# Optimization experiments

Measured on AMD Instinct MI355X. Metric: run time of the kernel, lower is better.

Reference implementation:

```python
import jax, jax.numpy as jnp
import numpy as np
from jax import lax

B, T, V, E, H, C, K = 256, 512, 50000, 128, 256, 128, 2


def setup_inputs() -> dict:
    key = jax.random.key(0)
    ks = jax.random.split(key, 16)
    s = lambda *sh: 1.0 / np.sqrt(sh[0])
    return {
        "input_current": jax.random.randint(ks[0], (B, T), 0, V, dtype=jnp.int32),
        "input_left": jax.random.randint(ks[1], (B, T), 0, V, dtype=jnp.int32),
        "input_right": jax.random.randint(ks[2], (B, T), 0, V, dtype=jnp.int32),
        "emb": jax.random.normal(ks[3], (V, E), jnp.float32) * 0.05,
        "Wf": jax.random.normal(ks[4], (E, H), jnp.float32) * s(E),
        "Uf": jax.random.normal(ks[5], (H, H), jnp.float32) * s(H),
        "bf": jnp.zeros((H,), jnp.float32),
        "Wb": jax.random.normal(ks[6], (E, H), jnp.float32) * s(E),
        "Ub": jax.random.normal(ks[7], (H, H), jnp.float32) * s(H),
        "bb": jnp.zeros((H,), jnp.float32),
        "Wc": jax.random.normal(ks[8], (2 * H + E, C), jnp.float32) * s(2 * H + E),
        "bc": jnp.zeros((C,), jnp.float32),
        "Wd": jax.random.normal(ks[9], (C, K), jnp.float32) * s(C),
        "bd": jnp.zeros((K,), jnp.float32),
    }


def _simple_rnn(x, W, U, b):
    # x: [B,T,E] -> outputs [B,T,H]; h_t = tanh(x_t W + b + h_{t-1} U)
    xw = jnp.einsum("bte,eh->bth", x, W) + b  # precompute input projection
    h0 = jnp.zeros((x.shape[0], U.shape[0]), x.dtype)

    def step(h, xw_t):
        h = jnp.tanh(xw_t + h @ U)
        return h, h

    _, hs = lax.scan(step, h0, jnp.swapaxes(xw, 0, 1))  # scan over time
    return jnp.swapaxes(hs, 0, 1)


def reference(input_current, input_left, input_right, emb, Wf, Uf, bf, Wb, Ub, bb, Wc, bc, Wd, bd):
    e_cur = emb[input_current]  # [B,T,E]
    e_left = emb[input_left]
    e_right = emb[input_right]
    x_left = _simple_rnn(e_left, Wf, Uf, bf)  # [B,T,H]
    # go_backwards RNN: process reversed sequence, then model reverses back
    x_right = _simple_rnn(e_right[:, ::-1], Wb, Ub, bb)[:, ::-1]  # [B,T,H]
    x = jnp.concatenate([x_left, e_cur, x_right], axis=2)  # [B,T,2H+E]
    x = jnp.tanh(jnp.einsum("btd,dc->btc", x, Wc) + bc)  # Conv1D k=1 + tanh
    x = jnp.max(x, axis=1)  # GlobalMaxPooling1D
    return jax.nn.sigmoid(x @ Wd + bd)  # [B,K]
```

## Files before the change

kernel.cpp:

```cpp
#include <hip/hip_runtime.h>
#include <hip/hip_bf16.h>


#define B_ 256
#define T_ 512
#define E_ 128
#define H_ 256
#define C_ 128

typedef __attribute__((ext_vector_type(8))) short short8;
typedef __attribute__((ext_vector_type(4))) float float4v;
typedef __attribute__((ext_vector_type(2))) unsigned int uint2v;

__device__ inline unsigned short f2bf(float f) {
  unsigned u = __float_as_uint(f);
  u += 0x7fffu + ((u >> 16) & 1u);
  return (unsigned short)(u >> 16);
}
__device__ inline unsigned pkbf(float a, float b) {
  __hip_bfloat162 h2 = __float22bfloat162_rn(float2{a, b});
  union { __hip_bfloat162 h; unsigned u; } cv;
  cv.h = h2;
  return cv.u;
}
__device__ inline float lo16f(unsigned u) { return __uint_as_float(u << 16); }
__device__ inline float hi16f(unsigned u) { return __uint_as_float(u & 0xffff0000u); }
__device__ inline float fast_tanh(float x) {
  float e = __expf(2.f * x);
  float r = __builtin_amdgcn_rcpf(e + 1.f);
  return __builtin_fmaf(-2.f, r, 1.f);
}
__device__ inline unsigned enc_f(float f) {
  unsigned u = __float_as_uint(f);
  return (u & 0x80000000u) ? ~u : (u | 0x80000000u);
}
__device__ inline float dec_f(unsigned key) {
  unsigned bits = (key & 0x80000000u) ? (key ^ 0x80000000u) : ~key;
  return __uint_as_float(bits);
}
__device__ inline void sync_lds() {
  asm volatile("s_waitcnt lgkmcnt(0)\n\ts_barrier" ::: "memory");
}

__global__ __launch_bounds__(256) void prep_kernel(
    const float* __restrict__ Wf, const float* __restrict__ Wb,
    const float* __restrict__ Wc, const float* __restrict__ Uf,
    const float* __restrict__ Ub,
    unsigned short* __restrict__ WfT, unsigned short* __restrict__ WbT,
    unsigned short* __restrict__ WcT, unsigned short* __restrict__ UfT,
    unsigned short* __restrict__ UbT) {
  int gid = blockIdx.x * 256 + threadIdx.x;
  int stride = gridDim.x * 256;
  for (int i = gid; i < 128 * 256; i += stride) {
    int k = i >> 8, n = i & 255;
    WfT[n * 128 + k] = f2bf(Wf[i]);
    WbT[n * 128 + k] = f2bf(Wb[i]);
  }
  for (int i = gid; i < 640 * 128; i += stride) {
    int k = i >> 7, n = i & 127;
    WcT[n * 640 + k] = f2bf(Wc[i]);
  }
  for (int i = gid; i < 256 * 256; i += stride) {
    int k = i >> 8, n = i & 255;
    UfT[n * 256 + k] = f2bf(Uf[i]);
    UbT[n * 256 + k] = f2bf(Ub[i]);
  }
}

__global__ __launch_bounds__(256) void embxw_kernel(
    const int* __restrict__ idxL, const int* __restrict__ idxR,
    const int* __restrict__ idxC, const float* __restrict__ emb,
    const unsigned short* __restrict__ WfT, const unsigned short* __restrict__ WbT,
    const float* __restrict__ bfv, const float* __restrict__ bbv,
    unsigned short* __restrict__ x) {
  const int dir = blockIdx.z;
  const int t0 = blockIdx.x * 4;
  const int b0 = blockIdx.y * 16;
  const int tid = threadIdx.x;
  const int w = tid >> 6, lane = tid & 63, q = lane >> 4, l15 = lane & 15;

  if (dir == 2) {
    const int t = t0 + w;
    const int er = idxC[(b0 + l15) * T_ + t];
    const float* ep = emb + (size_t)er * E_;
#pragma unroll
    for (int u = 0; u < 8; ++u) {
      float4v a = *(const float4v*)(ep + 16 * u + 4 * q);
      uint2v pk = {pkbf(a[0], a[1]), pkbf(a[2], a[3])};
      int row = b0 + u + 8 * (q >> 1);
      *(uint2v*)(x + ((size_t)row * T_ + t) * 640 + 256 + 64 * (q & 1) +
                 4 * l15) = pk;
    }
    return;
  }

  const int* __restrict__ idx = dir ? idxR : idxL;
  const unsigned short* __restrict__ WT = dir ? WbT : WfT;
  const float* __restrict__ bias = dir ? bbv : bfv;

  short8 wfr[4][4];
#pragma unroll
  for (int mt = 0; mt < 4; ++mt)
#pragma unroll
    for (int kt = 0; kt < 4; ++kt)
      wfr[mt][kt] = *(const short8*)(WT + (64 * w + 16 * mt + l15) * 128 +
                                     kt * 32 + q * 8);
  float4v bv[4];
#pragma unroll
  for (int mt = 0; mt < 4; ++mt)
    bv[mt] = *(const float4v*)(bias + 64 * w + 16 * mt + 4 * q);

#pragma unroll 1
  for (int j = 0; j < 4; ++j) {
    const int t = t0 + j;
    const int er = idx[(b0 + l15) * T_ + t];
    const float* ep = emb + (size_t)er * E_;
    short8 efr[4];
#pragma unroll
    for (int kt = 0; kt < 4; ++kt) {
      const float* p8 = ep + kt * 32 + q * 8;
      float4v a0 = *(const float4v*)p8;
      float4v a1 = *(const float4v*)(p8 + 4);
      union { unsigned u[4]; short8 s; } cv;
      cv.u[0] = pkbf(a0[0], a0[1]);
      cv.u[1] = pkbf(a0[2], a0[3]);
      cv.u[2] = pkbf(a1[0], a1[1]);
      cv.u[3] = pkbf(a1[2], a1[3]);
      efr[kt] = cv.s;
    }
    float4v acc[4];
#pragma unroll
    for (int mt = 0; mt < 4; ++mt) acc[mt] = (float4v){0.f, 0.f, 0.f, 0.f};
#pragma unroll
    for (int kt = 0; kt < 4; ++kt)
#pragma unroll
      for (int mt = 0; mt < 4; ++mt)
        acc[mt] = __builtin_amdgcn_mfma_f32_16x16x32_bf16(wfr[mt][kt], efr[kt],
                                                          acc[mt], 0, 0, 0);
#pragma unroll
    for (int mt = 0; mt < 4; ++mt) {
      float4v v = acc[mt] + bv[mt];
      uint2v pk = {pkbf(v[0], v[1]), pkbf(v[2], v[3])};
      *(uint2v*)(x + ((size_t)(b0 + 4 * w + mt) * T_ + t) * 640 + dir * 384 +
                 lane * 4) = pk;
    }
  }
}

__global__ __launch_bounds__(512, 2) void rnn_kernel(
    unsigned short* x, const unsigned short* __restrict__ UfT,
    const unsigned short* __restrict__ UbT) {
  const int dir = blockIdx.x & 1;
  const int b0 = (blockIdx.x >> 1) * 16;
  const unsigned short* __restrict__ UT = dir ? UbT : UfT;
  const int xoff = dir ? 384 : 0;
  const int tstep = dir ? -1 : 1;
  const int t0 = dir ? (T_ - 1) : 0;
  const ptrdiff_t dstep = (ptrdiff_t)tstep * 640;

  const int tid = threadIdx.x;
  const int wv = tid >> 6, lane = tid & 63, q = lane >> 4, l15 = lane & 15;

  __shared__ __attribute__((aligned(16))) unsigned short hbuf[2][16][280];
  unsigned short* hb0 = &hbuf[0][0][0];
  unsigned short* hb1 = &hbuf[1][0][0];

  for (int i = tid; i < 16 * 280; i += 512) hb0[i] = 0;

  short8 ufr[2][8];
#pragma unroll
  for (int mt = 0; mt < 2; ++mt)
#pragma unroll
    for (int kt = 0; kt < 8; ++kt)
      ufr[mt][kt] = *(const short8*)(UT + (32 * wv + 16 * mt + l15) * H_ +
                                     kt * 32 + q * 8);

  unsigned short* ptrS[2];
  const unsigned short* ptrL[2];
  uint2v curA[2], curB[2], infA[2], infB[2];
#pragma unroll
  for (int mt = 0; mt < 2; ++mt) {
    unsigned short* base =
        x + (size_t)(b0 + 2 * wv + mt) * T_ * 640 + xoff + lane * 4;
    unsigned short* bt = base + (ptrdiff_t)t0 * 640;
    curA[mt] = *(const uint2v*)(bt);
    curB[mt] = *(const uint2v*)(bt + dstep);
    infA[mt] = *(const uint2v*)(bt + 2 * dstep);
    infB[mt] = *(const uint2v*)(bt + 3 * dstep);
    ptrS[mt] = bt;
    ptrL[mt] = bt + 4 * dstep;
  }

  const unsigned lrd = l15 * 280;
  const unsigned lwr = l15 * 280 + 32 * wv;

  __syncthreads();

#pragma unroll 1
  for (int p = 0; p < 256; ++p) {
    uint2v ldA[2], ldB[2];
    if (p < 254) {
#pragma unroll
      for (int mt = 0; mt < 2; ++mt) {
        ldA[mt] = *(const uint2v*)(ptrL[mt]);
        ldB[mt] = *(const uint2v*)(ptrL[mt] + dstep);
      }
    } else {
#pragma unroll
      for (int mt = 0; mt < 2; ++mt) { ldA[mt] = infA[mt]; ldB[mt] = infB[mt]; }
    }
#pragma unroll
    for (int mt = 0; mt < 2; ++mt) ptrL[mt] += 2 * dstep;

    {
      short8 afr[8];
#pragma unroll
      for (int kt = 0; kt < 8; ++kt)
        afr[kt] = *(const short8*)(hb0 + lrd + kt * 32 + q * 8);
      float4v acc[2];
#pragma unroll
      for (int mt = 0; mt < 2; ++mt)
        acc[mt] = (float4v){lo16f(curA[mt].x), hi16f(curA[mt].x),
                            lo16f(curA[mt].y), hi16f(curA[mt].y)};
#pragma unroll
      for (int kt = 0; kt < 8; ++kt)
#pragma unroll
        for (int mt = 0; mt < 2; ++mt)
          acc[mt] = __builtin_amdgcn_mfma_f32_16x16x32_bf16(
              ufr[mt][kt], afr[kt], acc[mt], 0, 0, 0);
#pragma unroll
      for (int mt = 0; mt < 2; ++mt) {
        uint2v hv = {pkbf(fast_tanh(acc[mt][0]), fast_tanh(acc[mt][1])),
                     pkbf(fast_tanh(acc[mt][2]), fast_tanh(acc[mt][3]))};
        *(uint2v*)(hb1 + lwr + 16 * mt + 4 * q) = hv;
        *(uint2v*)ptrS[mt] = hv;
      }
    }
    sync_lds();

    {
      short8 afr[8];
#pragma unroll
      for (int kt = 0; kt < 8; ++kt)
        afr[kt] = *(const short8*)(hb1 + lrd + kt * 32 + q * 8);
      float4v acc[2];
#pragma unroll
      for (int mt = 0; mt < 2; ++mt)
        acc[mt] = (float4v){lo16f(curB[mt].x), hi16f(curB[mt].x),
                            lo16f(curB[mt].y), hi16f(curB[mt].y)};
#pragma unroll
      for (int kt = 0; kt < 8; ++kt)
#pragma unroll
        for (int mt = 0; mt < 2; ++mt)
          acc[mt] = __builtin_amdgcn_mfma_f32_16x16x32_bf16(
              ufr[mt][kt], afr[kt], acc[mt], 0, 0, 0);
#pragma unroll
      for (int mt = 0; mt < 2; ++mt) {
        uint2v hv = {pkbf(fast_tanh(acc[mt][0]), fast_tanh(acc[mt][1])),
                     pkbf(fast_tanh(acc[mt][2]), fast_tanh(acc[mt][3]))};
        *(uint2v*)(hb0 + lwr + 16 * mt + 4 * q) = hv;
        *(uint2v*)(ptrS[mt] + dstep) = hv;
      }
    }
#pragma unroll
    for (int mt = 0; mt < 2; ++mt) {
      ptrS[mt] += 2 * dstep;
      curA[mt] = infA[mt];
      curB[mt] = infB[mt];
      infA[mt] = ldA[mt];
      infB[mt] = ldB[mt];
    }
    sync_lds();
  }
}

__global__ __launch_bounds__(256, 2) void convpool_kernel(
    const unsigned short* __restrict__ x, const unsigned short* __restrict__ WcT,
    const float* __restrict__ bc, unsigned int* __restrict__ pooled) {
  const int b0 = (blockIdx.x & 15) * 16;
  const int t0 = (blockIdx.x >> 4) * 16;
  const int tid = threadIdx.x;
  const int w = tid >> 6, lane = tid & 63, q = lane >> 4, l15 = lane & 15;

  __shared__ __attribute__((aligned(16))) unsigned short tile[2][16][648];

  short8 wfr[2][20];
#pragma unroll
  for (int ct = 0; ct < 2; ++ct)
#pragma unroll
    for (int kt = 0; kt < 20; ++kt)
      wfr[ct][kt] = *(const short8*)(WcT +
                                     (size_t)(32 * w + 16 * ct + l15) * 640 +
                                     kt * 32 + q * 8);
  float4v bv[2];
#pragma unroll
  for (int ct = 0; ct < 2; ++ct)
    bv[ct] = *(const float4v*)(bc + 32 * w + 16 * ct + 4 * q);

  float4v mx[2];
  mx[0] = (float4v){-1e30f, -1e30f, -1e30f, -1e30f};
  mx[1] = mx[0];

  const int srow = tid >> 4, ssub = tid & 15;
  {
    const unsigned short* src = x + ((size_t)(b0 + srow) * T_ + t0) * 640;
#pragma unroll
    for (int j = 0; j < 5; ++j)
      *(short8*)&tile[0][srow][ssub * 8 + j * 128] =
          *(const short8*)(src + ssub * 8 + j * 128);
  }
  __syncthreads();

#pragma unroll 1
  for (int j = 0; j < 16; ++j) {
    const int t = t0 + j;
    const int buf = j & 1;
    if (j < 15) {
      const unsigned short* src = x + ((size_t)(b0 + srow) * T_ + t + 1) * 640;
#pragma unroll
      for (int jj = 0; jj < 5; ++jj)
        *(short8*)&tile[buf ^ 1][srow][ssub * 8 + jj * 128] =
            *(const short8*)(src + ssub * 8 + jj * 128);
    }
    float4v acc[2];
    acc[0] = (float4v){0.f, 0.f, 0.f, 0.f};
    acc[1] = (float4v){0.f, 0.f, 0.f, 0.f};
#pragma unroll
    for (int kt = 0; kt < 20; ++kt) {
      int row, so1, so2;
      if (kt < 8) {
        row = 2 * kt + (q >> 1);
        so1 = 64 * (2 * (q & 1)) + 4 * l15;
        so2 = so1 + 64;
      } else if (kt < 12) {
        row = 2 * (kt - 8) + (q >> 1) + 8 * (q & 1);
        so1 = 256 + 4 * l15;
        so2 = 320 + 4 * l15;
      } else {
        row = 2 * (kt - 12) + (q >> 1);
        so1 = 384 + 64 * (2 * (q & 1)) + 4 * l15;
        so2 = so1 + 64;
      }
      union { unsigned u[4]; short8 s; } cv;
      uint2v c1 = *(const uint2v*)&tile[buf][row][so1];
      uint2v c2 = *(const uint2v*)&tile[buf][row][so2];
      cv.u[0] = c1.x; cv.u[1] = c1.y; cv.u[2] = c2.x; cv.u[3] = c2.y;
      acc[0] = __builtin_amdgcn_mfma_f32_16x16x32_bf16(wfr[0][kt], cv.s,
                                                       acc[0], 0, 0, 0);
      acc[1] = __builtin_amdgcn_mfma_f32_16x16x32_bf16(wfr[1][kt], cv.s,
                                                       acc[1], 0, 0, 0);
    }
#pragma unroll
    for (int ct = 0; ct < 2; ++ct)
#pragma unroll
      for (int i = 0; i < 4; ++i)
        mx[ct][i] = fmaxf(mx[ct][i], acc[ct][i]);
    __syncthreads();
  }
#pragma unroll
  for (int ct = 0; ct < 2; ++ct)
#pragma unroll
    for (int i = 0; i < 4; ++i)
      atomicMax(pooled + (b0 + l15) * C_ + 32 * w + 16 * ct + 4 * q + i,
                enc_f(fast_tanh(mx[ct][i] + bv[ct][i])));
}

__global__ __launch_bounds__(256) void dense_kernel(
    const unsigned int* __restrict__ pooled, const float* __restrict__ Wd,
    const float* __restrict__ bd, float* __restrict__ out) {
  int b = threadIdx.x;
  float s0 = bd[0], s1 = bd[1];
#pragma unroll 4
  for (int c = 0; c < C_; ++c) {
    float f = dec_f(pooled[b * C_ + c]);
    s0 += f * Wd[c * 2 + 0];
    s1 += f * Wd[c * 2 + 1];
  }
  out[b * 2 + 0] = 1.f / (1.f + __expf(-s0));
  out[b * 2 + 1] = 1.f / (1.f + __expf(-s1));
}

extern "C" void kernel_launch(void* const* d_in, const int* in_sizes, int n_in,
                              void* d_out, int out_size, void* d_ws, size_t ws_size,
                              hipStream_t stream) {
  const int* idxC = (const int*)d_in[0];
  const int* idxL = (const int*)d_in[1];
  const int* idxR = (const int*)d_in[2];
  const float* emb = (const float*)d_in[3];
  const float* Wf = (const float*)d_in[4];
  const float* Uf = (const float*)d_in[5];
  const float* bf_ = (const float*)d_in[6];
  const float* Wb = (const float*)d_in[7];
  const float* Ub = (const float*)d_in[8];
  const float* bb_ = (const float*)d_in[9];
  const float* Wc = (const float*)d_in[10];
  const float* bc = (const float*)d_in[11];
  const float* Wd = (const float*)d_in[12];
  const float* bd = (const float*)d_in[13];

  char* ws = (char*)d_ws;
  unsigned short* x = (unsigned short*)ws;
  unsigned int* pooled = (unsigned int*)(ws + 167772160);
  unsigned short* WfT = (unsigned short*)(ws + 167772160 + 131072);
  unsigned short* WbT = WfT + 256 * 128;
  unsigned short* WcT = WbT + 256 * 128;
  unsigned short* UfT = WcT + 128 * 640;
  unsigned short* UbT = UfT + 256 * 256;

  hipMemsetAsync(pooled, 0, B_ * C_ * sizeof(unsigned int), stream);
  prep_kernel<<<64, 256, 0, stream>>>(Wf, Wb, Wc, Uf, Ub, WfT, WbT, WcT, UfT, UbT);
  embxw_kernel<<<dim3(128, 16, 3), 256, 0, stream>>>(idxL, idxR, idxC, emb,
                                                     WfT, WbT, bf_, bb_, x);
  rnn_kernel<<<32, 512, 0, stream>>>(x, UfT, UbT);
  convpool_kernel<<<512, 256, 0, stream>>>(x, WcT, bc, pooled);
  dense_kernel<<<1, 256, 0, stream>>>(pooled, Wd, bd, (float*)d_out);
}
```

Measured before the change: 629.8 us.

## Precompute vocab projections and fuse conv partial sums into the RNN loop

Projects the whole embedding table through Wf, Wb and the center slice of Wc once (V x 640 table), so the RNN gathers precomputed input projections by token index instead of reading a B x T x 640 activation buffer. The RNN kernel also applies its half of the Conv1D weights to each hidden state as it is produced and writes compact per-direction partial outputs. A lightweight pool kernel then sums the partials with the gathered center term, takes the max over time and applies tanh. This removes the large intermediate write and read and the separate conv GEMM, at the cost of a vocab-sized GEMM, extra MFMAs on the serial RNN critical path, and pre-activation partials rounded to bf16 before they are summed.

New measurement: 713.1 us. 13.2% more time.

```diff
diff --git a/kernel.cpp b/kernel.cpp
--- a/kernel.cpp
+++ b/kernel.cpp
@@ -7,6 +7,7 @@
 #define E_ 128
 #define H_ 256
 #define C_ 128
+#define V_ 50000
 
 typedef __attribute__((ext_vector_type(8))) short short8;
 typedef __attribute__((ext_vector_type(4))) float float4v;
@@ -41,122 +42,100 @@
 __device__ inline void sync_lds() {
   asm volatile("s_waitcnt lgkmcnt(0)\n\ts_barrier" ::: "memory");
 }
+__device__ inline int clampt(int t) { return t < 0 ? 0 : (t > 511 ? 511 : t); }
 
 __global__ __launch_bounds__(256) void prep_kernel(
     const float* __restrict__ Wf, const float* __restrict__ Wb,
     const float* __restrict__ Wc, const float* __restrict__ Uf,
-    const float* __restrict__ Ub,
-    unsigned short* __restrict__ WfT, unsigned short* __restrict__ WbT,
+    const float* __restrict__ Ub, const float* __restrict__ bf_,
+    const float* __restrict__ bb_,
+    unsigned short* __restrict__ WT_all, float* __restrict__ biasEW,
     unsigned short* __restrict__ WcT, unsigned short* __restrict__ UfT,
     unsigned short* __restrict__ UbT) {
   int gid = blockIdx.x * 256 + threadIdx.x;
   int stride = gridDim.x * 256;
   for (int i = gid; i < 128 * 256; i += stride) {
-    int k = i >> 8, n = i & 255;
-    WfT[n * 128 + k] = f2bf(Wf[i]);
-    WbT[n * 128 + k] = f2bf(Wb[i]);
+    int k = i >> 8, m = i & 255;
+    WT_all[m * 128 + k] = f2bf(Wf[i]);
+    WT_all[(256 + m) * 128 + k] = f2bf(Wb[i]);
   }
   for (int i = gid; i < 640 * 128; i += stride) {
-    int k = i >> 7, n = i & 127;
-    WcT[n * 640 + k] = f2bf(Wc[i]);
+    int d = i >> 7, c = i & 127;
+    unsigned short v = f2bf(Wc[i]);
+    WcT[c * 640 + d] = v;
+    if (d >= 256 && d < 384) WT_all[(512 + c) * 128 + (d - 256)] = v;
   }
   for (int i = gid; i < 256 * 256; i += stride) {
     int k = i >> 8, n = i & 255;
     UfT[n * 256 + k] = f2bf(Uf[i]);
     UbT[n * 256 + k] = f2bf(Ub[i]);
   }
-}
-
-__global__ __launch_bounds__(256) void embxw_kernel(
-    const int* __restrict__ idxL, const int* __restrict__ idxR,
-    const int* __restrict__ idxC, const float* __restrict__ emb,
-    const unsigned short* __restrict__ WfT, const unsigned short* __restrict__ WbT,
-    const float* __restrict__ bfv, const float* __restrict__ bbv,
-    unsigned short* __restrict__ x) {
-  const int dir = blockIdx.z;
-  const int t0 = blockIdx.x * 4;
-  const int b0 = blockIdx.y * 16;
+  for (int i = gid; i < 640; i += stride)
+    biasEW[i] = i < 256 ? bf_[i] : (i < 512 ? bb_[i - 256] : 0.f);
+}
+
+__global__ __launch_bounds__(256) void ew_kernel(
+    const float* __restrict__ emb, const unsigned short* __restrict__ WT_all,
+    const float* __restrict__ biasEW, unsigned short* __restrict__ EW) {
+  const int r0 = blockIdx.x * 16;
   const int tid = threadIdx.x;
   const int w = tid >> 6, lane = tid & 63, q = lane >> 4, l15 = lane & 15;
 
-  if (dir == 2) {
-    const int t = t0 + w;
-    const int er = idxC[(b0 + l15) * T_ + t];
-    const float* ep = emb + (size_t)er * E_;
-#pragma unroll
-    for (int u = 0; u < 8; ++u) {
-      float4v a = *(const float4v*)(ep + 16 * u + 4 * q);
-      uint2v pk = {pkbf(a[0], a[1]), pkbf(a[2], a[3])};
-      int row = b0 + u + 8 * (q >> 1);
-      *(uint2v*)(x + ((size_t)row * T_ + t) * 640 + 256 + 64 * (q & 1) +
-                 4 * l15) = pk;
-    }
-    return;
-  }
-
+  short8 wfr[10][4];
+#pragma unroll
+  for (int mt = 0; mt < 10; ++mt)
+#pragma unroll
+    for (int kt = 0; kt < 4; ++kt)
+      wfr[mt][kt] = *(const short8*)(WT_all + (160 * w + 16 * mt + l15) * 128 +
+                                     kt * 32 + q * 8);
+  short8 efr[4];
+#pragma unroll
+  for (int kt = 0; kt < 4; ++kt) {
+    const float* p8 = emb + (size_t)(r0 + l15) * E_ + kt * 32 + q * 8;
+    float4v a0 = *(const float4v*)p8;
+    float4v a1 = *(const float4v*)(p8 + 4);
+    union { unsigned u[4]; short8 s; } cv;
+    cv.u[0] = pkbf(a0[0], a0[1]);
+    cv.u[1] = pkbf(a0[2], a0[3]);
+    cv.u[2] = pkbf(a1[0], a1[1]);
+    cv.u[3] = pkbf(a1[2], a1[3]);
+    efr[kt] = cv.s;
+  }
+  float4v acc[10];
+#pragma unroll
+  for (int mt = 0; mt < 10; ++mt) acc[mt] = (float4v){0.f, 0.f, 0.f, 0.f};
+#pragma unroll
+  for (int kt = 0; kt < 4; ++kt)
+#pragma unroll
+    for (int mt = 0; mt < 10; ++mt)
+      acc[mt] = __builtin_amdgcn_mfma_f32_16x16x32_bf16(wfr[mt][kt], efr[kt],
+                                                        acc[mt], 0, 0, 0);
+#pragma unroll
+  for (int mt = 0; mt < 10; ++mt) {
+    const int col = 160 * w + 16 * mt + 4 * q;
+    float4v bv = *(const float4v*)(biasEW + col);
+    float4v v = acc[mt] + bv;
+    uint2v pk = {pkbf(v[0], v[1]), pkbf(v[2], v[3])};
+    *(uint2v*)(EW + (size_t)(r0 + l15) * 640 + col) = pk;
+  }
+}
+
+__global__ __launch_bounds__(512, 2) void rnn_kernel(
+    const int* __restrict__ idxL, const int* __restrict__ idxR,
+    const unsigned short* __restrict__ EW,
+    const unsigned short* __restrict__ UfT,
+    const unsigned short* __restrict__ UbT,
+    const unsigned short* __restrict__ WcT, unsigned short* __restrict__ pbuf) {
+  const int blk = blockIdx.x;
+  const int btile = blk & 15;
+  const int dir = blk >> 4;
+  const int b0 = btile * 16;
   const int* __restrict__ idx = dir ? idxR : idxL;
-  const unsigned short* __restrict__ WT = dir ? WbT : WfT;
-  const float* __restrict__ bias = dir ? bbv : bfv;
-
-  short8 wfr[4][4];
-#pragma unroll
-  for (int mt = 0; mt < 4; ++mt)
-#pragma unroll
-    for (int kt = 0; kt < 4; ++kt)
-      wfr[mt][kt] = *(const short8*)(WT + (64 * w + 16 * mt + l15) * 128 +
-                                     kt * 32 + q * 8);
-  float4v bv[4];
-#pragma unroll
-  for (int mt = 0; mt < 4; ++mt)
-    bv[mt] = *(const float4v*)(bias + 64 * w + 16 * mt + 4 * q);
-
-#pragma unroll 1
-  for (int j = 0; j < 4; ++j) {
-    const int t = t0 + j;
-    const int er = idx[(b0 + l15) * T_ + t];
-    const float* ep = emb + (size_t)er * E_;
-    short8 efr[4];
-#pragma unroll
-    for (int kt = 0; kt < 4; ++kt) {
-      const float* p8 = ep + kt * 32 + q * 8;
-      float4v a0 = *(const float4v*)p8;
-      float4v a1 = *(const float4v*)(p8 + 4);
-      union { unsigned u[4]; short8 s; } cv;
-      cv.u[0] = pkbf(a0[0], a0[1]);
-      cv.u[1] = pkbf(a0[2], a0[3]);
-      cv.u[2] = pkbf(a1[0], a1[1]);
-      cv.u[3] = pkbf(a1[2], a1[3]);
-      efr[kt] = cv.s;
-    }
-    float4v acc[4];
-#pragma unroll
-    for (int mt = 0; mt < 4; ++mt) acc[mt] = (float4v){0.f, 0.f, 0.f, 0.f};
-#pragma unroll
-    for (int kt = 0; kt < 4; ++kt)
-#pragma unroll
-      for (int mt = 0; mt < 4; ++mt)
-        acc[mt] = __builtin_amdgcn_mfma_f32_16x16x32_bf16(wfr[mt][kt], efr[kt],
-                                                          acc[mt], 0, 0, 0);
-#pragma unroll
-    for (int mt = 0; mt < 4; ++mt) {
-      float4v v = acc[mt] + bv[mt];
-      uint2v pk = {pkbf(v[0], v[1]), pkbf(v[2], v[3])};
-      *(uint2v*)(x + ((size_t)(b0 + 4 * w + mt) * T_ + t) * 640 + dir * 384 +
-                 lane * 4) = pk;
-    }
-  }
-}
-
-__global__ __launch_bounds__(512, 2) void rnn_kernel(
-    unsigned short* x, const unsigned short* __restrict__ UfT,
-    const unsigned short* __restrict__ UbT) {
-  const int dir = blockIdx.x & 1;
-  const int b0 = (blockIdx.x >> 1) * 16;
   const unsigned short* __restrict__ UT = dir ? UbT : UfT;
-  const int xoff = dir ? 384 : 0;
+  const int ewoff = dir ? 256 : 0;
+  const int wcoff = dir ? 384 : 0;
   const int tstep = dir ? -1 : 1;
-  const int t0 = dir ? (T_ - 1) : 0;
-  const ptrdiff_t dstep = (ptrdiff_t)tstep * 640;
+  const int tstart = dir ? (T_ - 1) : 0;
 
   const int tid = threadIdx.x;
   const int wv = tid >> 6, lane = tid & 63, q = lane >> 4, l15 = lane & 15;
@@ -164,7 +143,6 @@
   __shared__ __attribute__((aligned(16))) unsigned short hbuf[2][16][280];
   unsigned short* hb0 = &hbuf[0][0][0];
   unsigned short* hb1 = &hbuf[1][0][0];
-
   for (int i = tid; i < 16 * 280; i += 512) hb0[i] = 0;
 
   short8 ufr[2][8];
@@ -174,49 +152,61 @@
     for (int kt = 0; kt < 8; ++kt)
       ufr[mt][kt] = *(const short8*)(UT + (32 * wv + 16 * mt + l15) * H_ +
                                      kt * 32 + q * 8);
-
-  unsigned short* ptrS[2];
-  const unsigned short* ptrL[2];
-  uint2v curA[2], curB[2], infA[2], infB[2];
+  short8 wcfr[8];
+#pragma unroll
+  for (int kt = 0; kt < 8; ++kt)
+    wcfr[kt] = *(const short8*)(WcT + (size_t)(16 * wv + l15) * 640 + wcoff +
+                                kt * 32 + q * 8);
+
+  const int idxbase = (b0 + l15) * T_;
+  const int eofs = ewoff + 32 * wv + 4 * q;
+
+  int i0A = idx[idxbase + tstart];
+  int i0B = idx[idxbase + tstart + tstep];
+  int ihA = idx[idxbase + tstart + 2 * tstep];
+  int ihB = idx[idxbase + tstart + 3 * tstep];
+  uint2v curA[2], curB[2];
 #pragma unroll
   for (int mt = 0; mt < 2; ++mt) {
-    unsigned short* base =
-        x + (size_t)(b0 + 2 * wv + mt) * T_ * 640 + xoff + lane * 4;
-    unsigned short* bt = base + (ptrdiff_t)t0 * 640;
-    curA[mt] = *(const uint2v*)(bt);
-    curB[mt] = *(const uint2v*)(bt + dstep);
-    infA[mt] = *(const uint2v*)(bt + 2 * dstep);
-    infB[mt] = *(const uint2v*)(bt + 3 * dstep);
-    ptrS[mt] = bt;
-    ptrL[mt] = bt + 4 * dstep;
-  }
+    curA[mt] = *(const uint2v*)(EW + (size_t)i0A * 640 + eofs + 16 * mt);
+    curB[mt] = *(const uint2v*)(EW + (size_t)i0B * 640 + eofs + 16 * mt);
+  }
+
+  unsigned short* pwbase =
+      pbuf + ((size_t)(dir * 128 + btile * 8 + wv) * T_) * 256 + 64 * q +
+      4 * l15;
 
   const unsigned lrd = l15 * 280;
   const unsigned lwr = l15 * 280 + 32 * wv;
 
   __syncthreads();
 
+  int tA = tstart;
 #pragma unroll 1
   for (int p = 0; p < 256; ++p) {
-    uint2v ldA[2], ldB[2];
-    if (p < 254) {
-#pragma unroll
-      for (int mt = 0; mt < 2; ++mt) {
-        ldA[mt] = *(const uint2v*)(ptrL[mt]);
-        ldB[mt] = *(const uint2v*)(ptrL[mt] + dstep);
-      }
-    } else {
-#pragma unroll
-      for (int mt = 0; mt < 2; ++mt) { ldA[mt] = infA[mt]; ldB[mt] = infB[mt]; }
-    }
-#pragma unroll
-    for (int mt = 0; mt < 2; ++mt) ptrL[mt] += 2 * dstep;
+    int ilA = idx[idxbase + clampt(tA + 4 * tstep)];
+    int ilB = idx[idxbase + clampt(tA + 5 * tstep)];
+    uint2v nxtA[2], nxtB[2];
+#pragma unroll
+    for (int mt = 0; mt < 2; ++mt) {
+      nxtA[mt] = *(const uint2v*)(EW + (size_t)ihA * 640 + eofs + 16 * mt);
+      nxtB[mt] = *(const uint2v*)(EW + (size_t)ihB * 640 + eofs + 16 * mt);
+    }
 
     {
       short8 afr[8];
 #pragma unroll
       for (int kt = 0; kt < 8; ++kt)
         afr[kt] = *(const short8*)(hb0 + lrd + kt * 32 + q * 8);
+      if (p >= 1) {
+        float4v pacc = (float4v){0.f, 0.f, 0.f, 0.f};
+#pragma unroll
+        for (int kt = 0; kt < 8; ++kt)
+          pacc = __builtin_amdgcn_mfma_f32_16x16x32_bf16(wcfr[kt], afr[kt],
+                                                         pacc, 0, 0, 0);
+        uint2v pk = {pkbf(pacc[0], pacc[1]), pkbf(pacc[2], pacc[3])};
+        *(uint2v*)(pwbase + (tA - tstep) * 256) = pk;
+      }
       float4v acc[2];
 #pragma unroll
       for (int mt = 0; mt < 2; ++mt)
@@ -233,7 +223,6 @@
         uint2v hv = {pkbf(fast_tanh(acc[mt][0]), fast_tanh(acc[mt][1])),
                      pkbf(fast_tanh(acc[mt][2]), fast_tanh(acc[mt][3]))};
         *(uint2v*)(hb1 + lwr + 16 * mt + 4 * q) = hv;
-        *(uint2v*)ptrS[mt] = hv;
       }
     }
     sync_lds();
@@ -243,6 +232,15 @@
 #pragma unroll
       for (int kt = 0; kt < 8; ++kt)
         afr[kt] = *(const short8*)(hb1 + lrd + kt * 32 + q * 8);
+      {
+        float4v pacc = (float4v){0.f, 0.f, 0.f, 0.f};
+#pragma unroll
+        for (int kt = 0; kt < 8; ++kt)
+          pacc = __builtin_amdgcn_mfma_f32_16x16x32_bf16(wcfr[kt], afr[kt],
+                                                         pacc, 0, 0, 0);
+        uint2v pk = {pkbf(pacc[0], pacc[1]), pkbf(pacc[2], pacc[3])};
+        *(uint2v*)(pwbase + tA * 256) = pk;
+      }
       float4v acc[2];
 #pragma unroll
       for (int mt = 0; mt < 2; ++mt)
@@ -259,110 +257,83 @@
         uint2v hv = {pkbf(fast_tanh(acc[mt][0]), fast_tanh(acc[mt][1])),
                      pkbf(fast_tanh(acc[mt][2]), fast_tanh(acc[mt][3]))};
         *(uint2v*)(hb0 + lwr + 16 * mt + 4 * q) = hv;
-        *(uint2v*)(ptrS[mt] + dstep) = hv;
       }
     }
 #pragma unroll
     for (int mt = 0; mt < 2; ++mt) {
-      ptrS[mt] += 2 * dstep;
-      curA[mt] = infA[mt];
-      curB[mt] = infB[mt];
-      infA[mt] = ldA[mt];
-      infB[mt] = ldB[mt];
-    }
+      curA[mt] = nxtA[mt];
+      curB[mt] = nxtB[mt];
+    }
+    ihA = ilA;
+    ihB = ilB;
+    tA += 2 * tstep;
     sync_lds();
   }
-}
-
-__global__ __launch_bounds__(256, 2) void convpool_kernel(
-    const unsigned short* __restrict__ x, const unsigned short* __restrict__ WcT,
-    const float* __restrict__ bc, unsigned int* __restrict__ pooled) {
-  const int b0 = (blockIdx.x & 15) * 16;
-  const int t0 = (blockIdx.x >> 4) * 16;
+
+  {
+    short8 afr[8];
+#pragma unroll
+    for (int kt = 0; kt < 8; ++kt)
+      afr[kt] = *(const short8*)(hb0 + lrd + kt * 32 + q * 8);
+    float4v pacc = (float4v){0.f, 0.f, 0.f, 0.f};
+#pragma unroll
+    for (int kt = 0; kt < 8; ++kt)
+      pacc = __builtin_amdgcn_mfma_f32_16x16x32_bf16(wcfr[kt], afr[kt], pacc,
+                                                     0, 0, 0);
+    uint2v pk = {pkbf(pacc[0], pacc[1]), pkbf(pacc[2], pacc[3])};
+    *(uint2v*)(pwbase + (tA - tstep) * 256) = pk;
+  }
+}
+
+__global__ __launch_bounds__(256) void pool_kernel(
+    const int* __restrict__ idxC, const unsigned short* __restrict__ EW,
+    const unsigned short* __restrict__ pbuf, const float* __restrict__ bc,
+    unsigned int* __restrict__ pooled) {
+  const int btile = blockIdx.x & 15;
+  const int tch = blockIdx.x >> 4;
+  const int b0 = btile * 16;
   const int tid = threadIdx.x;
   const int w = tid >> 6, lane = tid & 63, q = lane >> 4, l15 = lane & 15;
-
-  __shared__ __attribute__((aligned(16))) unsigned short tile[2][16][648];
-
-  short8 wfr[2][20];
-#pragma unroll
-  for (int ct = 0; ct < 2; ++ct)
-#pragma unroll
-    for (int kt = 0; kt < 20; ++kt)
-      wfr[ct][kt] = *(const short8*)(WcT +
-                                     (size_t)(32 * w + 16 * ct + l15) * 640 +
-                                     kt * 32 + q * 8);
-  float4v bv[2];
-#pragma unroll
-  for (int ct = 0; ct < 2; ++ct)
-    bv[ct] = *(const float4v*)(bc + 32 * w + 16 * ct + 4 * q);
-
-  float4v mx[2];
-  mx[0] = (float4v){-1e30f, -1e30f, -1e30f, -1e30f};
-  mx[1] = mx[0];
-
-  const int srow = tid >> 4, ssub = tid & 15;
-  {
-    const unsigned short* src = x + ((size_t)(b0 + srow) * T_ + t0) * 640;
-#pragma unroll
-    for (int j = 0; j < 5; ++j)
-      *(short8*)&tile[0][srow][ssub * 8 + j * 128] =
-          *(const short8*)(src + ssub * 8 + j * 128);
-  }
-  __syncthreads();
-
-#pragma unroll 1
-  for (int j = 0; j < 16; ++j) {
-    const int t = t0 + j;
-    const int buf = j & 1;
-    if (j < 15) {
-      const unsigned short* src = x + ((size_t)(b0 + srow) * T_ + t + 1) * 640;
-#pragma unroll
-      for (int jj = 0; jj < 5; ++jj)
-        *(short8*)&tile[buf ^ 1][srow][ssub * 8 + jj * 128] =
-            *(const short8*)(src + ssub * 8 + jj * 128);
-    }
-    float4v acc[2];
-    acc[0] = (float4v){0.f, 0.f, 0.f, 0.f};
-    acc[1] = (float4v){0.f, 0.f, 0.f, 0.f};
-#pragma unroll
-    for (int kt = 0; kt < 20; ++kt) {
-      int row, so1, so2;
-      if (kt < 8) {
-        row = 2 * kt + (q >> 1);
-        so1 = 64 * (2 * (q & 1)) + 4 * l15;
-        so2 = so1 + 64;
-      } else if (kt < 12) {
-        row = 2 * (kt - 8) + (q >> 1) + 8 * (q & 1);
-        so1 = 256 + 4 * l15;
-        so2 = 320 + 4 * l15;
-      } else {
-        row = 2 * (kt - 12) + (q >> 1);
-        so1 = 384 + 64 * (2 * (q & 1)) + 4 * l15;
-        so2 = so1 + 64;
-      }
-      union { unsigned u[4]; short8 s; } cv;
-      uint2v c1 = *(const uint2v*)&tile[buf][row][so1];
-      uint2v c2 = *(const uint2v*)&tile[buf][row][so2];
-      cv.u[0] = c1.x; cv.u[1] = c1.y; cv.u[2] = c2.x; cv.u[3] = c2.y;
-      acc[0] = __builtin_amdgcn_mfma_f32_16x16x32_bf16(wfr[0][kt], cv.s,
-                                                       acc[0], 0, 0, 0);
-      acc[1] = __builtin_amdgcn_mfma_f32_16x16x32_bf16(wfr[1][kt], cv.s,
-                                                       acc[1], 0, 0, 0);
-    }
-#pragma unroll
-    for (int ct = 0; ct < 2; ++ct)
-#pragma unroll
-      for (int i = 0; i < 4; ++i)
-        mx[ct][i] = fmaxf(mx[ct][i], acc[ct][i]);
-    __syncthreads();
-  }
-#pragma unroll
-  for (int ct = 0; ct < 2; ++ct)
+  const int loff = 64 * q + 4 * l15;
+
+  float4v mx[8];
+#pragma unroll
+  for (int u = 0; u < 8; ++u)
+    mx[u] = (float4v){-1e30f, -1e30f, -1e30f, -1e30f};
+
+#pragma unroll 2
+  for (int j = 0; j < 8; ++j) {
+    const int t = tch * 32 + w * 8 + j;
+    const int row = idxC[(b0 + l15) * T_ + t];
+    const unsigned short* ecp = EW + (size_t)row * 640 + 512 + 4 * q;
+#pragma unroll
+    for (int u = 0; u < 8; ++u) {
+      uint2v pf = *(const uint2v*)(pbuf +
+                                   ((size_t)(btile * 8 + u) * T_ + t) * 256 +
+                                   loff);
+      uint2v pb = *(const uint2v*)(pbuf +
+                                   ((size_t)(128 + btile * 8 + u) * T_ + t) *
+                                       256 +
+                                   loff);
+      uint2v ec = *(const uint2v*)(ecp + 16 * u);
+      float v0 = lo16f(pf.x) + lo16f(pb.x) + lo16f(ec.x);
+      float v1 = hi16f(pf.x) + hi16f(pb.x) + hi16f(ec.x);
+      float v2 = lo16f(pf.y) + lo16f(pb.y) + lo16f(ec.y);
+      float v3 = hi16f(pf.y) + hi16f(pb.y) + hi16f(ec.y);
+      mx[u][0] = fmaxf(mx[u][0], v0);
+      mx[u][1] = fmaxf(mx[u][1], v1);
+      mx[u][2] = fmaxf(mx[u][2], v2);
+      mx[u][3] = fmaxf(mx[u][3], v3);
+    }
+  }
+#pragma unroll
+  for (int u = 0; u < 8; ++u) {
+    float4v bcv = *(const float4v*)(bc + 16 * u + 4 * q);
 #pragma unroll
     for (int i = 0; i < 4; ++i)
-      atomicMax(pooled + (b0 + l15) * C_ + 32 * w + 16 * ct + 4 * q + i,
-                enc_f(fast_tanh(mx[ct][i] + bv[ct][i])));
+      atomicMax(pooled + (b0 + l15) * C_ + 16 * u + 4 * q + i,
+                enc_f(fast_tanh(mx[u][i] + bcv[i])));
+  }
 }
 
 __global__ __launch_bounds__(256) void dense_kernel(
@@ -399,19 +370,20 @@
   const float* bd = (const float*)d_in[13];
 
   char* ws = (char*)d_ws;
-  unsigned short* x = (unsigned short*)ws;
-  unsigned int* pooled = (unsigned int*)(ws + 167772160);
-  unsigned short* WfT = (unsigned short*)(ws + 167772160 + 131072);
-  unsigned short* WbT = WfT + 256 * 128;
-  unsigned short* WcT = WbT + 256 * 128;
-  unsigned short* UfT = WcT + 128 * 640;
-  unsigned short* UbT = UfT + 256 * 256;
+  unsigned short* EW = (unsigned short*)ws;
+  unsigned short* pbuf = (unsigned short*)(ws + 64000000);
+  unsigned int* pooled = (unsigned int*)(ws + 131108864);
+  unsigned short* WT_all = (unsigned short*)(ws + 131239936);
+  float* biasEW = (float*)(ws + 131403776);
+  unsigned short* WcT = (unsigned short*)(ws + 131406336);
+  unsigned short* UfT = (unsigned short*)(ws + 131570176);
+  unsigned short* UbT = (unsigned short*)(ws + 131701248);
 
   hipMemsetAsync(pooled, 0, B_ * C_ * sizeof(unsigned int), stream);
-  prep_kernel<<<64, 256, 0, stream>>>(Wf, Wb, Wc, Uf, Ub, WfT, WbT, WcT, UfT, UbT);
-  embxw_kernel<<<dim3(128, 16, 3), 256, 0, stream>>>(idxL, idxR, idxC, emb,
-                                                     WfT, WbT, bf_, bb_, x);
-  rnn_kernel<<<32, 512, 0, stream>>>(x, UfT, UbT);
-  convpool_kernel<<<512, 256, 0, stream>>>(x, WcT, bc, pooled);
+  prep_kernel<<<64, 256, 0, stream>>>(Wf, Wb, Wc, Uf, Ub, bf_, bb_, WT_all,
+                                      biasEW, WcT, UfT, UbT);
+  ew_kernel<<<V_ / 16, 256, 0, stream>>>(emb, WT_all, biasEW, EW);
+  rnn_kernel<<<32, 512, 0, stream>>>(idxL, idxR, EW, UfT, UbT, WcT, pbuf);
+  pool_kernel<<<256, 256, 0, stream>>>(idxC, EW, pbuf, bc, pooled);
   dense_kernel<<<1, 256, 0, stream>>>(pooled, Wd, bd, (float*)d_out);
 }
```

## Precompute emb·Wc_mid per vocab row and split x buffer into compact per-direction layout

Applied to the files above, without the earlier changes.

The centre-embedding slice of the conv weight is applied to the whole vocabulary table once (50000x128 by 128x128) instead of storing gathered embeddings per (b,t) and multiplying them in convpool. Convpool now gathers the precomputed row through idxC and adds it to the MFMA result over the two hidden-state halves, which cuts its K dimension from 640 to 512. The intermediate buffer becomes two separate [B,T,256] arrays, dropping the 640-wide interleaved layout and the embedding copy writes. The cost is an extra vocabulary-sized GEMM and a random gather per timestep, plus one more bf16 rounding on the centre term.

Result: slower. 689.6 us (+9.5%).

```diff
diff --git a/kernel.cpp b/kernel.cpp
--- a/kernel.cpp
+++ b/kernel.cpp
@@ -7,6 +7,7 @@
 #define E_ 128
 #define H_ 256
 #define C_ 128
+#define V_ 50000
 
 typedef __attribute__((ext_vector_type(8))) short short8;
 typedef __attribute__((ext_vector_type(4))) float float4v;
@@ -69,30 +70,15 @@
 
 __global__ __launch_bounds__(256) void embxw_kernel(
     const int* __restrict__ idxL, const int* __restrict__ idxR,
-    const int* __restrict__ idxC, const float* __restrict__ emb,
+    const float* __restrict__ emb,
     const unsigned short* __restrict__ WfT, const unsigned short* __restrict__ WbT,
     const float* __restrict__ bfv, const float* __restrict__ bbv,
-    unsigned short* __restrict__ x) {
+    unsigned short* __restrict__ xwh) {
   const int dir = blockIdx.z;
   const int t0 = blockIdx.x * 4;
   const int b0 = blockIdx.y * 16;
   const int tid = threadIdx.x;
   const int w = tid >> 6, lane = tid & 63, q = lane >> 4, l15 = lane & 15;
-
-  if (dir == 2) {
-    const int t = t0 + w;
-    const int er = idxC[(b0 + l15) * T_ + t];
-    const float* ep = emb + (size_t)er * E_;
-#pragma unroll
-    for (int u = 0; u < 8; ++u) {
-      float4v a = *(const float4v*)(ep + 16 * u + 4 * q);
-      uint2v pk = {pkbf(a[0], a[1]), pkbf(a[2], a[3])};
-      int row = b0 + u + 8 * (q >> 1);
-      *(uint2v*)(x + ((size_t)row * T_ + t) * 640 + 256 + 64 * (q & 1) +
-                 4 * l15) = pk;
-    }
-    return;
-  }
 
   const int* __restrict__ idx = dir ? idxR : idxL;
   const unsigned short* __restrict__ WT = dir ? WbT : WfT;
@@ -141,22 +127,67 @@
     for (int mt = 0; mt < 4; ++mt) {
       float4v v = acc[mt] + bv[mt];
       uint2v pk = {pkbf(v[0], v[1]), pkbf(v[2], v[3])};
-      *(uint2v*)(x + ((size_t)(b0 + 4 * w + mt) * T_ + t) * 640 + dir * 384 +
+      *(uint2v*)(xwh +
+                 ((size_t)(dir * 256 + b0 + 4 * w + mt) * T_ + t) * 256 +
                  lane * 4) = pk;
     }
   }
 }
 
+__global__ __launch_bounds__(256) void ewmid_kernel(
+    const float* __restrict__ emb, const unsigned short* __restrict__ WcT,
+    unsigned short* __restrict__ ECmid) {
+  const int r0 = blockIdx.x * 16;
+  const int tid = threadIdx.x;
+  const int w = tid >> 6, lane = tid & 63, q = lane >> 4, l15 = lane & 15;
+
+  short8 wfr[2][4];
+#pragma unroll
+  for (int mt = 0; mt < 2; ++mt)
+#pragma unroll
+    for (int kt = 0; kt < 4; ++kt)
+      wfr[mt][kt] = *(const short8*)(WcT +
+                                     (size_t)(32 * w + 16 * mt + l15) * 640 +
+                                     256 + kt * 32 + q * 8);
+  short8 efr[4];
+#pragma unroll
+  for (int kt = 0; kt < 4; ++kt) {
+    const float* p8 = emb + (size_t)(r0 + l15) * E_ + kt * 32 + q * 8;
+    float4v a0 = *(const float4v*)p8;
+    float4v a1 = *(const float4v*)(p8 + 4);
+    union { unsigned u[4]; short8 s; } cv;
+    cv.u[0] = pkbf(a0[0], a0[1]);
+    cv.u[1] = pkbf(a0[2], a0[3]);
+    cv.u[2] = pkbf(a1[0], a1[1]);
+    cv.u[3] = pkbf(a1[2], a1[3]);
+    efr[kt] = cv.s;
+  }
+  float4v acc[2];
+  acc[0] = (float4v){0.f, 0.f, 0.f, 0.f};
+  acc[1] = (float4v){0.f, 0.f, 0.f, 0.f};
+#pragma unroll
+  for (int kt = 0; kt < 4; ++kt)
+#pragma unroll
+    for (int mt = 0; mt < 2; ++mt)
+      acc[mt] = __builtin_amdgcn_mfma_f32_16x16x32_bf16(wfr[mt][kt], efr[kt],
+                                                        acc[mt], 0, 0, 0);
+#pragma unroll
+  for (int mt = 0; mt < 2; ++mt) {
+    uint2v pk = {pkbf(acc[mt][0], acc[mt][1]), pkbf(acc[mt][2], acc[mt][3])};
+    *(uint2v*)(ECmid + (size_t)(r0 + l15) * 128 + 32 * w + 16 * mt + 4 * q) =
+        pk;
+  }
+}
+
 __global__ __launch_bounds__(512, 2) void rnn_kernel(
-    unsigned short* x, const unsigned short* __restrict__ UfT,
+    unsigned short* xwh, const unsigned short* __restrict__ UfT,
     const unsigned short* __restrict__ UbT) {
   const int dir = blockIdx.x & 1;
   const int b0 = (blockIdx.x >> 1) * 16;
   const unsigned short* __restrict__ UT = dir ? UbT : UfT;
-  const int xoff = dir ? 384 : 0;
   const int tstep = dir ? -1 : 1;
   const int t0 = dir ? (T_ - 1) : 0;
-  const ptrdiff_t dstep = (ptrdiff_t)tstep * 640;
+  const ptrdiff_t dstep = (ptrdiff_t)tstep * 256;
 
   const int tid = threadIdx.x;
   const int wv = tid >> 6, lane = tid & 63, q = lane >> 4, l15 = lane & 15;
@@ -181,8 +212,8 @@
 #pragma unroll
   for (int mt = 0; mt < 2; ++mt) {
     unsigned short* base =
-        x + (size_t)(b0 + 2 * wv + mt) * T_ * 640 + xoff + lane * 4;
-    unsigned short* bt = base + (ptrdiff_t)t0 * 640;
+        xwh + (size_t)(dir * 256 + b0 + 2 * wv + mt) * T_ * 256 + lane * 4;
+    unsigned short* bt = base + (ptrdiff_t)t0 * 256;
     curA[mt] = *(const uint2v*)(bt);
     curB[mt] = *(const uint2v*)(bt + dstep);
     infA[mt] = *(const uint2v*)(bt + 2 * dstep);
@@ -275,94 +306,95 @@
 }
 
 __global__ __launch_bounds__(256, 2) void convpool_kernel(
-    const unsigned short* __restrict__ x, const unsigned short* __restrict__ WcT,
-    const float* __restrict__ bc, unsigned int* __restrict__ pooled) {
-  const int b0 = (blockIdx.x & 15) * 16;
-  const int t0 = (blockIdx.x >> 4) * 16;
+    const int* __restrict__ idxC, const unsigned short* __restrict__ xwh,
+    const unsigned short* __restrict__ ECmid,
+    const unsigned short* __restrict__ WcT, const float* __restrict__ bc,
+    unsigned int* __restrict__ pooled) {
+  const int btile = blockIdx.x & 15;
+  const int tch = blockIdx.x >> 4;
+  const int b0 = btile * 16;
+  const int t0 = tch * 16;
   const int tid = threadIdx.x;
   const int w = tid >> 6, lane = tid & 63, q = lane >> 4, l15 = lane & 15;
 
-  __shared__ __attribute__((aligned(16))) unsigned short tile[2][16][648];
-
-  short8 wfr[2][20];
-#pragma unroll
-  for (int ct = 0; ct < 2; ++ct)
-#pragma unroll
-    for (int kt = 0; kt < 20; ++kt)
-      wfr[ct][kt] = *(const short8*)(WcT +
-                                     (size_t)(32 * w + 16 * ct + l15) * 640 +
-                                     kt * 32 + q * 8);
+  __shared__ __attribute__((aligned(16))) unsigned short tile[2][32][258];
+
+  short8 wfr[2][16];
+#pragma unroll
+  for (int mt = 0; mt < 2; ++mt)
+#pragma unroll
+    for (int kt = 0; kt < 16; ++kt) {
+      const int krow = kt < 8 ? kt * 32 : 384 + (kt - 8) * 32;
+      wfr[mt][kt] = *(const short8*)(WcT +
+                                     (size_t)(32 * w + 16 * mt + l15) * 640 +
+                                     krow + q * 8);
+    }
   float4v bv[2];
 #pragma unroll
-  for (int ct = 0; ct < 2; ++ct)
-    bv[ct] = *(const float4v*)(bc + 32 * w + 16 * ct + 4 * q);
+  for (int mt = 0; mt < 2; ++mt)
+    bv[mt] = *(const float4v*)(bc + 32 * w + 16 * mt + 4 * q);
 
   float4v mx[2];
   mx[0] = (float4v){-1e30f, -1e30f, -1e30f, -1e30f};
   mx[1] = mx[0];
 
-  const int srow = tid >> 4, ssub = tid & 15;
-  {
-    const unsigned short* src = x + ((size_t)(b0 + srow) * T_ + t0) * 640;
-#pragma unroll
-    for (int j = 0; j < 5; ++j)
-      *(short8*)&tile[0][srow][ssub * 8 + j * 128] =
-          *(const short8*)(src + ssub * 8 + j * 128);
-  }
-  __syncthreads();
+  const int su = tid >> 3, ssub = tid & 7;
+  const int srow = su < 16 ? (b0 + su) : (256 + b0 + su - 16);
+  const unsigned short* sbase = xwh + (size_t)srow * T_ * 256 + ssub * 8;
+
+#pragma unroll
+  for (int j2 = 0; j2 < 4; ++j2)
+    *(short8*)&tile[0][su][ssub * 8 + j2 * 64] =
+        *(const short8*)(sbase + (size_t)t0 * 256 + j2 * 64);
+  sync_lds();
 
 #pragma unroll 1
   for (int j = 0; j < 16; ++j) {
     const int t = t0 + j;
     const int buf = j & 1;
     if (j < 15) {
-      const unsigned short* src = x + ((size_t)(b0 + srow) * T_ + t + 1) * 640;
-#pragma unroll
-      for (int jj = 0; jj < 5; ++jj)
-        *(short8*)&tile[buf ^ 1][srow][ssub * 8 + jj * 128] =
-            *(const short8*)(src + ssub * 8 + jj * 128);
-    }
+#pragma unroll
+      for (int j2 = 0; j2 < 4; ++j2)
+        *(short8*)&tile[buf ^ 1][su][ssub * 8 + j2 * 64] =
+            *(const short8*)(sbase + (size_t)(t + 1) * 256 + j2 * 64);
+    }
+    const int erow = idxC[(b0 + l15) * T_ + t];
+    uint2v ec[2];
+#pragma unroll
+    for (int mt = 0; mt < 2; ++mt)
+      ec[mt] = *(const uint2v*)(ECmid + (size_t)erow * 128 + 32 * w +
+                                16 * mt + 4 * q);
     float4v acc[2];
     acc[0] = (float4v){0.f, 0.f, 0.f, 0.f};
     acc[1] = (float4v){0.f, 0.f, 0.f, 0.f};
 #pragma unroll
-    for (int kt = 0; kt < 20; ++kt) {
-      int row, so1, so2;
-      if (kt < 8) {
-        row = 2 * kt + (q >> 1);
-        so1 = 64 * (2 * (q & 1)) + 4 * l15;
-        so2 = so1 + 64;
-      } else if (kt < 12) {
-        row = 2 * (kt - 8) + (q >> 1) + 8 * (q & 1);
-        so1 = 256 + 4 * l15;
-        so2 = 320 + 4 * l15;
-      } else {
-        row = 2 * (kt - 12) + (q >> 1);
-        so1 = 384 + 64 * (2 * (q & 1)) + 4 * l15;
-        so2 = so1 + 64;
-      }
-      union { unsigned u[4]; short8 s; } cv;
-      uint2v c1 = *(const uint2v*)&tile[buf][row][so1];
-      uint2v c2 = *(const uint2v*)&tile[buf][row][so2];
-      cv.u[0] = c1.x; cv.u[1] = c1.y; cv.u[2] = c2.x; cv.u[3] = c2.y;
+    for (int kt = 0; kt < 16; ++kt) {
+      const int u = 2 * (kt & 7) + (q >> 1) + ((kt >= 8) ? 16 : 0);
+      const unsigned short* tb = &tile[buf][u][128 * (q & 1) + 4 * l15];
+      uint2v c1 = *(const uint2v*)tb;
+      uint2v c2 = *(const uint2v*)(tb + 64);
+      union { unsigned uu[4]; short8 s; } cv;
+      cv.uu[0] = c1.x; cv.uu[1] = c1.y; cv.uu[2] = c2.x; cv.uu[3] = c2.y;
       acc[0] = __builtin_amdgcn_mfma_f32_16x16x32_bf16(wfr[0][kt], cv.s,
                                                        acc[0], 0, 0, 0);
       acc[1] = __builtin_amdgcn_mfma_f32_16x16x32_bf16(wfr[1][kt], cv.s,
                                                        acc[1], 0, 0, 0);
     }
 #pragma unroll
-    for (int ct = 0; ct < 2; ++ct)
-#pragma unroll
-      for (int i = 0; i < 4; ++i)
-        mx[ct][i] = fmaxf(mx[ct][i], acc[ct][i]);
-    __syncthreads();
-  }
-#pragma unroll
-  for (int ct = 0; ct < 2; ++ct)
+    for (int mt = 0; mt < 2; ++mt) {
+      float4v v = acc[mt] + (float4v){lo16f(ec[mt].x), hi16f(ec[mt].x),
+                                      lo16f(ec[mt].y), hi16f(ec[mt].y)};
+#pragma unroll
+      for (int i = 0; i < 4; ++i) mx[mt][i] = fmaxf(mx[mt][i], v[i]);
+    }
+    sync_lds();
+  }
+#pragma unroll
+  for (int mt = 0; mt < 2; ++mt)
 #pragma unroll
     for (int i = 0; i < 4; ++i)
-      atomicMax(pooled + (b0 + l15) * C_ + 32 * w + 16 * ct + 4 * q + i,
-                enc_f(fast_tanh(mx[ct][i] + bv[ct][i])));
+      atomicMax(pooled + (b0 + l15) * C_ + 32 * w + 16 * mt + 4 * q + i,
+                enc_f(fast_tanh(mx[mt][i] + bv[mt][i])));
 }
 
 __global__ __launch_bounds__(256) void dense_kernel(
@@ -399,19 +431,22 @@
   const float* bd = (const float*)d_in[13];
 
   char* ws = (char*)d_ws;
-  unsigned short* x = (unsigned short*)ws;
-  unsigned int* pooled = (unsigned int*)(ws + 167772160);
-  unsigned short* WfT = (unsigned short*)(ws + 167772160 + 131072);
-  unsigned short* WbT = WfT + 256 * 128;
-  unsigned short* WcT = WbT + 256 * 128;
-  unsigned short* UfT = WcT + 128 * 640;
-  unsigned short* UbT = UfT + 256 * 256;
+  unsigned short* xwh = (unsigned short*)ws;
+  unsigned short* ECmid = (unsigned short*)(ws + 134217728);
+  unsigned int* pooled = (unsigned int*)(ws + 147017728);
+  unsigned short* WfT = (unsigned short*)(ws + 147148800);
+  unsigned short* WbT = (unsigned short*)(ws + 147214336);
+  unsigned short* WcT = (unsigned short*)(ws + 147279872);
+  unsigned short* UfT = (unsigned short*)(ws + 147443712);
+  unsigned short* UbT = (unsigned short*)(ws + 147574784);
 
   hipMemsetAsync(pooled, 0, B_ * C_ * sizeof(unsigned int), stream);
-  prep_kernel<<<64, 256, 0, stream>>>(Wf, Wb, Wc, Uf, Ub, WfT, WbT, WcT, UfT, UbT);
-  embxw_kernel<<<dim3(128, 16, 3), 256, 0, stream>>>(idxL, idxR, idxC, emb,
-                                                     WfT, WbT, bf_, bb_, x);
-  rnn_kernel<<<32, 512, 0, stream>>>(x, UfT, UbT);
-  convpool_kernel<<<512, 256, 0, stream>>>(x, WcT, bc, pooled);
+  prep_kernel<<<64, 256, 0, stream>>>(Wf, Wb, Wc, Uf, Ub, WfT, WbT, WcT, UfT,
+                                      UbT);
+  embxw_kernel<<<dim3(128, 16, 2), 256, 0, stream>>>(idxL, idxR, emb, WfT,
+                                                     WbT, bf_, bb_, xwh);
+  ewmid_kernel<<<V_ / 16, 256, 0, stream>>>(emb, WcT, ECmid);
+  rnn_kernel<<<32, 512, 0, stream>>>(xwh, UfT, UbT);
+  convpool_kernel<<<512, 256, 0, stream>>>(idxC, xwh, ECmid, WcT, bc, pooled);
   dense_kernel<<<1, 256, 0, stream>>>(pooled, Wd, bd, (float*)d_out);
 }
```
